# Performance work log

Hardware: AMD Instinct MI355X
Metric: run time of the kernel (lower is better)

## Reference

```python
import jax, jax.numpy as jnp
import numpy as np

N_NODES = 100000
N_EDGES = 3200000
D_FEAT = 512
HIDDEN = 16
N_CLASSES = 7


def setup_inputs() -> dict:
    key = jax.random.key(0)
    k1, k2, k3, k4 = jax.random.split(key, 4)
    x = jax.random.normal(k1, (N_NODES, D_FEAT), dtype=jnp.float32)
    edge_index = jax.random.randint(k2, (2, N_EDGES), 0, N_NODES, dtype=jnp.int64)
    # Glorot-ish scaled weights
    W1 = jax.random.normal(k3, (D_FEAT, HIDDEN), dtype=jnp.float32) * (1.0 / np.sqrt(D_FEAT))
    b1 = jnp.zeros((HIDDEN,), dtype=jnp.float32)
    W2 = jax.random.normal(k4, (HIDDEN, N_CLASSES), dtype=jnp.float32) * (1.0 / np.sqrt(HIDDEN))
    b2 = jnp.zeros((N_CLASSES,), dtype=jnp.float32)
    return {"x": x, "edge_index": edge_index, "W1": W1, "b1": b1, "W2": W2, "b2": b2}


def _gcn_norm(edge_index, num_nodes):
    # Add self-loops, then symmetric normalization: D^-1/2 A D^-1/2
    loop = jnp.arange(num_nodes, dtype=edge_index.dtype)
    src = jnp.concatenate([edge_index[0], loop])
    dst = jnp.concatenate([edge_index[1], loop])
    deg = jax.ops.segment_sum(jnp.ones_like(dst, dtype=jnp.float32), dst,
                              num_segments=num_nodes)
    dinv = jnp.where(deg > 0, jax.lax.rsqrt(deg), 0.0)
    w = dinv[src] * dinv[dst]  # [E+N]
    return src, dst, w


def _gcn_conv(x, W, b, src, dst, w, num_nodes):
    h = x @ W                               # transform first (small out dim)
    m = jax.ops.segment_sum(h[src] * w[:, None], dst, num_segments=num_nodes)
    return m + b


def reference(x, edge_index, W1, b1, W2, b2):
    n = x.shape[0]
    src, dst, w = _gcn_norm(edge_index, n)
    h = jax.nn.relu(_gcn_conv(x, W1, b1, src, dst, w, n))
    # dropout is identity at inference
    logits = _gcn_conv(h, W2, b2, src, dst, w, n)
    return jax.nn.log_softmax(logits, axis=1)
```

## Files before the change

### kernel.cpp

```cpp
#include <hip/hip_runtime.h>
#include <cmath>

#define N_NODES   100000
#define N_EDGES   3200000
#define D_FEAT    512
#define HIDDEN    16
#define N_CLASSES 7

#define NCHUNK 250
#define CHUNK  12800
#define NBKT   1563
#define NSCAN  (NBKT * NCHUNK)

typedef __attribute__((ext_vector_type(4))) float  f32x4;
typedef __attribute__((ext_vector_type(8))) short  bf16x8;

__device__ __forceinline__ short f2bf(float f) {
    union { float f; unsigned u; } v; v.f = f;
    unsigned r = v.u + 0x7fffu + ((v.u >> 16) & 1u);
    return (short)(r >> 16);
}
__device__ __forceinline__ float bf2f(unsigned short s) {
    union { unsigned u; float f; } v; v.u = ((unsigned)s) << 16;
    return v.f;
}

__global__ __launch_bounds__(1024) void k_hist1(const int* __restrict__ dst,
                                                unsigned* __restrict__ hist) {
    __shared__ unsigned h[NBKT];
    int t = threadIdx.x, b = blockIdx.x;
    for (int i = t; i < NBKT; i += 1024) h[i] = 0u;
    __syncthreads();
    int base = b * CHUNK;
    #pragma unroll 2
    for (int k = 0; k < 13; ++k) {
        int idx = k * 1024 + t;
        if (idx < CHUNK) atomicAdd(&h[((unsigned)dst[base + idx]) >> 6], 1u);
    }
    __syncthreads();
    for (int i = t; i < NBKT; i += 1024)
        hist[(size_t)i * NCHUNK + b] = h[i];
}

__global__ __launch_bounds__(256) void k_scan_a(unsigned* __restrict__ hist,
                                                unsigned* __restrict__ bin_total) {
    __shared__ unsigned t0[256];
    int t = threadIdx.x, b = blockIdx.x;
    unsigned v = (t < NCHUNK) ? hist[(size_t)b * NCHUNK + t] : 0u;
    t0[t] = v; __syncthreads();
    #pragma unroll
    for (int off = 1; off < 256; off <<= 1) {
        unsigned add = (t >= off) ? t0[t - off] : 0u;
        __syncthreads();
        t0[t] += add;
        __syncthreads();
    }
    if (t < NCHUNK) hist[(size_t)b * NCHUNK + t] = t0[t] - v;
    if (t == 255) bin_total[b] = t0[t];
}

__global__ __launch_bounds__(256) void k_scan_b(const unsigned* __restrict__ bin_total,
                                                unsigned* __restrict__ bin_base) {
    __shared__ unsigned t0[256];
    int t = threadIdx.x;
    unsigned running = 0u;
    for (int c0 = 0; c0 < NBKT; c0 += 256) {
        int i = c0 + t;
        unsigned v = (i < NBKT) ? bin_total[i] : 0u;
        t0[t] = v; __syncthreads();
        #pragma unroll
        for (int off = 1; off < 256; off <<= 1) {
            unsigned add = (t >= off) ? t0[t - off] : 0u;
            __syncthreads();
            t0[t] += add;
            __syncthreads();
        }
        if (i < NBKT) bin_base[i] = running + t0[t] - v;
        unsigned chunk_sum = t0[255];
        __syncthreads();
        running += chunk_sum;
    }
    if (t == 0) bin_base[NBKT] = running;
}

__global__ __launch_bounds__(1024) void k_scatter1(const int* __restrict__ src,
                                                   const int* __restrict__ dst,
                                                   const unsigned* __restrict__ hist,
                                                   const unsigned* __restrict__ bin_base,
                                                   unsigned* __restrict__ packed) {
    __shared__ unsigned cur[NBKT];
    int t = threadIdx.x, b = blockIdx.x;
    for (int i = t; i < NBKT; i += 1024)
        cur[i] = hist[(size_t)i * NCHUNK + b] + bin_base[i];
    __syncthreads();
    int base = b * CHUNK;
    #pragma unroll 2
    for (int k = 0; k < 13; ++k) {
        int idx = k * 1024 + t;
        if (idx < CHUNK) {
            int e = base + idx;
            unsigned d = (unsigned)dst[e];
            unsigned pos = atomicAdd(&cur[d >> 6], 1u);
            packed[pos] = ((d & 63u) << 24) | (unsigned)src[e];
        }
    }
}

__global__ __launch_bounds__(256) void k_bucket(const unsigned* __restrict__ packed,
                                                const unsigned* __restrict__ bin_base,
                                                unsigned* __restrict__ deg,
                                                unsigned* __restrict__ row_start,
                                                float* __restrict__ dinv,
                                                int* __restrict__ csr_src) {
    __shared__ unsigned hh[4][64], sc[64], cur[64];
    int t = threadIdx.x, b = blockIdx.x;
    int w = t >> 6, l = t & 63;
    unsigned rs = bin_base[b];
    unsigned re = bin_base[b + 1];
    hh[w][l] = 0u;
    __syncthreads();
    for (unsigned i = rs + t; i < re; i += 256)
        atomicAdd(&hh[w][packed[i] >> 24], 1u);
    __syncthreads();
    unsigned total = 0u;
    if (t < 64) {
        total = hh[0][t] + hh[1][t] + hh[2][t] + hh[3][t];
        sc[t] = total;
    }
    __syncthreads();
    #pragma unroll
    for (int off = 1; off < 64; off <<= 1) {
        unsigned add = (t >= off && t < 64) ? sc[t - off] : 0u;
        __syncthreads();
        if (t < 64) sc[t] += add;
        __syncthreads();
    }
    if (t < 64) {
        unsigned excl = sc[t] - total;
        int node = b * 64 + t;
        if (node < N_NODES) {
            deg[node]       = total;
            row_start[node] = rs + excl;
            dinv[node]      = rsqrtf((float)(total + 1u));
        }
        cur[t] = rs + excl;
    }
    __syncthreads();
    for (unsigned i = rs + t; i < re; i += 256) {
        unsigned p = packed[i];
        unsigned pos = atomicAdd(&cur[p >> 24], 1u);
        csr_src[pos] = (int)(p & 0xFFFFFFu);
    }
}

__global__ __launch_bounds__(256) void k_gemm1(const float* __restrict__ x,
                                               const float* __restrict__ w1,
                                               const float* __restrict__ dinv,
                                               unsigned short* __restrict__ h1p) {
    __shared__ __align__(16) short w1t[16][520];
    int tid = threadIdx.x;
    for (int idx = tid; idx < D_FEAT * HIDDEN; idx += 256) {
        int k = idx >> 4, n = idx & 15;
        w1t[n][k] = f2bf(w1[idx]);
    }
    __syncthreads();

    int lane = tid & 63, wid = tid >> 6;
    int m  = lane & 15;
    int kg = lane >> 4;

    bf16x8 bfrag[16];
    #pragma unroll
    for (int ks = 0; ks < 16; ++ks)
        bfrag[ks] = *(const bf16x8*)&w1t[m][ks * 32 + kg * 8];

    int tile = blockIdx.x * 4 + wid;
    if (tile >= (N_NODES / 16)) return;

    const f32x4* xr = (const f32x4*)(x + (size_t)(tile * 16 + m) * D_FEAT);
    f32x4 acc = {0.f, 0.f, 0.f, 0.f};
    #pragma unroll
    for (int ks = 0; ks < 16; ++ks) {
        f32x4 x0 = xr[ks * 8 + kg * 2];
        f32x4 x1 = xr[ks * 8 + kg * 2 + 1];
        bf16x8 a;
        a[0] = f2bf(x0[0]); a[1] = f2bf(x0[1]); a[2] = f2bf(x0[2]); a[3] = f2bf(x0[3]);
        a[4] = f2bf(x1[0]); a[5] = f2bf(x1[1]); a[6] = f2bf(x1[2]); a[7] = f2bf(x1[3]);
        acc = __builtin_amdgcn_mfma_f32_16x16x32_bf16(a, bfrag[ks], acc, 0, 0, 0);
    }
    size_t base = (size_t)tile * 256;
    #pragma unroll
    for (int r = 0; r < 4; ++r) {
        int rr = kg * 4 + r;
        h1p[base + rr * 16 + m] = (unsigned short)f2bf(dinv[tile * 16 + rr] * acc[r]);
    }
}

__global__ __launch_bounds__(256) void k_gather1(const int* __restrict__ csr_src,
                                                 const unsigned* __restrict__ row_start,
                                                 const unsigned* __restrict__ deg,
                                                 const unsigned short* __restrict__ h1p,
                                                 float* __restrict__ g1) {
    int tid  = threadIdx.x;
    int lane = tid & 63;
    int node = blockIdx.x * 4 + (tid >> 6);
    int j  = lane & 15;
    int sl = lane >> 4;

    unsigned start = row_start[node];
    unsigned end   = start + deg[node];

    float acc = (sl == 0) ? bf2f(h1p[(size_t)node * 16 + j]) : 0.f;
    unsigned e = start;
    for (; e + 16 <= end; e += 16) {
        int s0 = csr_src[e      + sl];
        int s1 = csr_src[e + 4  + sl];
        int s2 = csr_src[e + 8  + sl];
        int s3 = csr_src[e + 12 + sl];
        float v0 = bf2f(h1p[(size_t)s0 * 16 + j]);
        float v1 = bf2f(h1p[(size_t)s1 * 16 + j]);
        float v2 = bf2f(h1p[(size_t)s2 * 16 + j]);
        float v3 = bf2f(h1p[(size_t)s3 * 16 + j]);
        acc += v0; acc += v1; acc += v2; acc += v3;
    }
    for (; e < end; e += 4) {
        unsigned idx = e + (unsigned)sl;
        float v = 0.f;
        if (idx < end) v = bf2f(h1p[(size_t)csr_src[idx] * 16 + j]);
        acc += v;
    }
    acc += __shfl_down(acc, 32);
    acc += __shfl_down(acc, 16);
    if (sl == 0) g1[(size_t)node * 16 + j] = acc;
}

__global__ __launch_bounds__(256) void k_layer2(const float* __restrict__ g1,
                                                const float* __restrict__ dinv,
                                                const float* __restrict__ w2,
                                                const float* __restrict__ b1,
                                                float* __restrict__ h2p) {
    int i = blockIdx.x * 256 + threadIdx.x;
    if (i >= N_NODES) return;
    float di = dinv[i];
    const float* gr = g1 + (size_t)i * 16;
    float h[16];
    #pragma unroll
    for (int j = 0; j < 16; ++j) h[j] = fmaxf(di * gr[j] + b1[j], 0.f);
    float* h2r = h2p + (size_t)i * 8;
    #pragma unroll
    for (int c = 0; c < N_CLASSES; ++c) {
        float o = 0.f;
        #pragma unroll
        for (int j = 0; j < 16; ++j) o += h[j] * w2[j * N_CLASSES + c];
        h2r[c] = di * o;
    }
    h2r[7] = 0.f;
}

__global__ __launch_bounds__(256) void k_gather2(const int* __restrict__ csr_src,
                                                 const unsigned* __restrict__ row_start,
                                                 const unsigned* __restrict__ deg,
                                                 const float* __restrict__ dinv,
                                                 const float* __restrict__ h2p,
                                                 const float* __restrict__ b2,
                                                 float* __restrict__ out) {
    int tid  = threadIdx.x;
    int lane = tid & 63;
    int node = blockIdx.x * 4 + (tid >> 6);
    int j  = lane & 7;
    int sl = lane >> 3;

    unsigned start = row_start[node];
    unsigned end   = start + deg[node];

    float acc = (sl == 0) ? h2p[(size_t)node * 8 + j] : 0.f;
    unsigned e = start;
    for (; e + 32 <= end; e += 32) {
        int s0 = csr_src[e      + sl];
        int s1 = csr_src[e + 8  + sl];
        int s2 = csr_src[e + 16 + sl];
        int s3 = csr_src[e + 24 + sl];
        float v0 = h2p[(size_t)s0 * 8 + j];
        float v1 = h2p[(size_t)s1 * 8 + j];
        float v2 = h2p[(size_t)s2 * 8 + j];
        float v3 = h2p[(size_t)s3 * 8 + j];
        acc += v0; acc += v1; acc += v2; acc += v3;
    }
    for (; e < end; e += 8) {
        unsigned idx = e + (unsigned)sl;
        float v = 0.f;
        if (idx < end) v = h2p[(size_t)csr_src[idx] * 8 + j];
        acc += v;
    }
    acc += __shfl_down(acc, 32);
    acc += __shfl_down(acc, 16);
    acc += __shfl_down(acc, 8);
    float di = dinv[node];
    float logit = (j < N_CLASSES) ? di * acc + b2[j] : -1e30f;
    float mx = logit;
    #pragma unroll
    for (int mk = 1; mk < 8; mk <<= 1) mx = fmaxf(mx, __shfl_xor(mx, mk, 8));
    float ex = (j < N_CLASSES) ? __expf(logit - mx) : 0.f;
    float sum = ex;
    #pragma unroll
    for (int mk = 1; mk < 8; mk <<= 1) sum += __shfl_xor(sum, mk, 8);
    if (sl == 0 && j < N_CLASSES)
        out[(size_t)node * N_CLASSES + j] = logit - mx - __logf(sum);
}

extern "C" void kernel_launch(void* const* d_in, const int* in_sizes, int n_in,
                              void* d_out, int out_size, void* d_ws, size_t ws_size,
                              hipStream_t stream) {
    const float* x  = (const float*)d_in[0];
    const int*   ei = (const int*)d_in[1];
    const float* w1 = (const float*)d_in[2];
    const float* b1 = (const float*)d_in[3];
    const float* w2 = (const float*)d_in[4];
    const float* b2 = (const float*)d_in[5];
    float* out = (float*)d_out;

    const int* src = ei;
    const int* dst = ei + N_EDGES;

    unsigned* w32        = (unsigned*)d_ws;
    float*    dinv       = (float*)(w32 + 0);
    unsigned short* h1p  = (unsigned short*)(w32 + 102400);
    float*    g1         = (float*)(w32 + 902400);
    float*    h2p        = (float*)(w32 + 2502400);
    unsigned* deg        = w32 + 3302400;
    unsigned* row_start  = w32 + 3404800;
    unsigned* hist       = w32 + 3507200;
    unsigned* bin_total  = w32 + 3897984;
    unsigned* bin_base   = w32 + 3899552;
    unsigned* packed     = w32 + 3901120;
    int*      csr_src    = (int*)(w32 + 7101120);

    const int GB = (N_NODES / 16 + 3) / 4;

    k_hist1   <<<NCHUNK, 1024, 0, stream>>>(dst, hist);
    k_scan_a  <<<NBKT,   256,  0, stream>>>(hist, bin_total);
    k_scan_b  <<<1,      256,  0, stream>>>(bin_total, bin_base);
    k_scatter1<<<NCHUNK, 1024, 0, stream>>>(src, dst, hist, bin_base, packed);
    k_bucket  <<<NBKT,   256,  0, stream>>>(packed, bin_base, deg, row_start, dinv, csr_src);
    k_gemm1   <<<GB,     256,  0, stream>>>(x, w1, dinv, h1p);
    k_gather1 <<<25000,  256,  0, stream>>>(csr_src, row_start, deg, h1p, g1);
    k_layer2  <<<(N_NODES + 255) / 256, 256, 0, stream>>>(g1, dinv, w2, b1, h2p);
    k_gather2 <<<25000,  256,  0, stream>>>(csr_src, row_start, deg, dinv, h2p, b2, out);
}
```

Measured before the change: 490.8 us.

## Fuse layer-2 transform into gather1, store h2 as bf16, stage bucket in LDS

Folds the per-node ReLU and W2 projection into the first gather kernel, using a 16-lane shuffle reduction, and removes the separate k_layer2 launch along with the g1 intermediate. h2 is now written as packed bf16 (16 bytes per node), which halves the bytes gathered in the second aggregation at some cost in precision. k_bucket copies its bucket's packed entries into shared memory once instead of reading global memory twice. The gather loops drop their separate tail loops in favour of predicated full iterations.

Result: slower. 528.1 us (+7.6%).

```diff
diff --git a/kernel.cpp b/kernel.cpp
--- a/kernel.cpp
+++ b/kernel.cpp
@@ -10,7 +10,7 @@
 #define NCHUNK 250
 #define CHUNK  12800
 #define NBKT   1563
-#define NSCAN  (NBKT * NCHUNK)
+#define BCAP   4096
 
 typedef __attribute__((ext_vector_type(4))) float  f32x4;
 typedef __attribute__((ext_vector_type(8))) short  bf16x8;
@@ -112,15 +112,22 @@
                                                 unsigned* __restrict__ row_start,
                                                 float* __restrict__ dinv,
                                                 int* __restrict__ csr_src) {
+    __shared__ unsigned pbuf[BCAP];
     __shared__ unsigned hh[4][64], sc[64], cur[64];
     int t = threadIdx.x, b = blockIdx.x;
     int w = t >> 6, l = t & 63;
     unsigned rs = bin_base[b];
     unsigned re = bin_base[b + 1];
+    unsigned n  = re - rs;
+    bool fits = (n <= BCAP);
+    if (fits)
+        for (unsigned i = t; i < n; i += 256) pbuf[i] = packed[rs + i];
     hh[w][l] = 0u;
     __syncthreads();
-    for (unsigned i = rs + t; i < re; i += 256)
-        atomicAdd(&hh[w][packed[i] >> 24], 1u);
+    for (unsigned i = t; i < n; i += 256) {
+        unsigned p = fits ? pbuf[i] : packed[rs + i];
+        atomicAdd(&hh[w][p >> 24], 1u);
+    }
     __syncthreads();
     unsigned total = 0u;
     if (t < 64) {
@@ -146,8 +153,8 @@
         cur[t] = rs + excl;
     }
     __syncthreads();
-    for (unsigned i = rs + t; i < re; i += 256) {
-        unsigned p = packed[i];
+    for (unsigned i = t; i < n; i += 256) {
+        unsigned p = fits ? pbuf[i] : packed[rs + i];
         unsigned pos = atomicAdd(&cur[p >> 24], 1u);
         csr_src[pos] = (int)(p & 0xFFFFFFu);
     }
@@ -199,69 +206,68 @@
 __global__ __launch_bounds__(256) void k_gather1(const int* __restrict__ csr_src,
                                                  const unsigned* __restrict__ row_start,
                                                  const unsigned* __restrict__ deg,
+                                                 const float* __restrict__ dinv,
                                                  const unsigned short* __restrict__ h1p,
-                                                 float* __restrict__ g1) {
+                                                 const float* __restrict__ w2,
+                                                 const float* __restrict__ b1,
+                                                 unsigned short* __restrict__ h2p) {
     int tid  = threadIdx.x;
     int lane = tid & 63;
     int node = blockIdx.x * 4 + (tid >> 6);
     int j  = lane & 15;
     int sl = lane >> 4;
 
+    float b1j = b1[j];
+    float w2j[N_CLASSES];
+    #pragma unroll
+    for (int c = 0; c < N_CLASSES; ++c) w2j[c] = w2[j * N_CLASSES + c];
+
     unsigned start = row_start[node];
     unsigned end   = start + deg[node];
 
     float acc = (sl == 0) ? bf2f(h1p[(size_t)node * 16 + j]) : 0.f;
-    unsigned e = start;
-    for (; e + 16 <= end; e += 16) {
-        int s0 = csr_src[e      + sl];
-        int s1 = csr_src[e + 4  + sl];
-        int s2 = csr_src[e + 8  + sl];
-        int s3 = csr_src[e + 12 + sl];
-        float v0 = bf2f(h1p[(size_t)s0 * 16 + j]);
-        float v1 = bf2f(h1p[(size_t)s1 * 16 + j]);
-        float v2 = bf2f(h1p[(size_t)s2 * 16 + j]);
-        float v3 = bf2f(h1p[(size_t)s3 * 16 + j]);
+    for (unsigned e0 = start; e0 < end; e0 += 16) {
+        unsigned i0 = e0 + (unsigned)sl, i1 = i0 + 4, i2 = i0 + 8, i3 = i0 + 12;
+        int s0 = (i0 < end) ? csr_src[i0] : 0;
+        int s1 = (i1 < end) ? csr_src[i1] : 0;
+        int s2 = (i2 < end) ? csr_src[i2] : 0;
+        int s3 = (i3 < end) ? csr_src[i3] : 0;
+        float v0 = (i0 < end) ? bf2f(h1p[(size_t)s0 * 16 + j]) : 0.f;
+        float v1 = (i1 < end) ? bf2f(h1p[(size_t)s1 * 16 + j]) : 0.f;
+        float v2 = (i2 < end) ? bf2f(h1p[(size_t)s2 * 16 + j]) : 0.f;
+        float v3 = (i3 < end) ? bf2f(h1p[(size_t)s3 * 16 + j]) : 0.f;
         acc += v0; acc += v1; acc += v2; acc += v3;
-    }
-    for (; e < end; e += 4) {
-        unsigned idx = e + (unsigned)sl;
-        float v = 0.f;
-        if (idx < end) v = bf2f(h1p[(size_t)csr_src[idx] * 16 + j]);
-        acc += v;
     }
     acc += __shfl_down(acc, 32);
     acc += __shfl_down(acc, 16);
-    if (sl == 0) g1[(size_t)node * 16 + j] = acc;
-}
-
-__global__ __launch_bounds__(256) void k_layer2(const float* __restrict__ g1,
-                                                const float* __restrict__ dinv,
-                                                const float* __restrict__ w2,
-                                                const float* __restrict__ b1,
-                                                float* __restrict__ h2p) {
-    int i = blockIdx.x * 256 + threadIdx.x;
-    if (i >= N_NODES) return;
-    float di = dinv[i];
-    const float* gr = g1 + (size_t)i * 16;
-    float h[16];
-    #pragma unroll
-    for (int j = 0; j < 16; ++j) h[j] = fmaxf(di * gr[j] + b1[j], 0.f);
-    float* h2r = h2p + (size_t)i * 8;
-    #pragma unroll
-    for (int c = 0; c < N_CLASSES; ++c) {
-        float o = 0.f;
+    float di = dinv[node];
+    float h = fmaxf(di * acc + b1j, 0.f);
+    float s[N_CLASSES];
+    #pragma unroll
+    for (int c = 0; c < N_CLASSES; ++c) s[c] = h * w2j[c];
+    #pragma unroll
+    for (int mk = 1; mk < 16; mk <<= 1) {
         #pragma unroll
-        for (int j = 0; j < 16; ++j) o += h[j] * w2[j * N_CLASSES + c];
-        h2r[c] = di * o;
-    }
-    h2r[7] = 0.f;
+        for (int c = 0; c < N_CLASSES; ++c) s[c] += __shfl_xor(s[c], mk, 16);
+    }
+    if (lane == 0) {
+        unsigned u0 = (unsigned)(unsigned short)f2bf(di * s[0]) |
+                      ((unsigned)(unsigned short)f2bf(di * s[1]) << 16);
+        unsigned u1 = (unsigned)(unsigned short)f2bf(di * s[2]) |
+                      ((unsigned)(unsigned short)f2bf(di * s[3]) << 16);
+        unsigned u2 = (unsigned)(unsigned short)f2bf(di * s[4]) |
+                      ((unsigned)(unsigned short)f2bf(di * s[5]) << 16);
+        unsigned u3 = (unsigned)(unsigned short)f2bf(di * s[6]);
+        uint4 pk; pk.x = u0; pk.y = u1; pk.z = u2; pk.w = u3;
+        *(uint4*)(h2p + (size_t)node * 8) = pk;
+    }
 }
 
 __global__ __launch_bounds__(256) void k_gather2(const int* __restrict__ csr_src,
                                                  const unsigned* __restrict__ row_start,
                                                  const unsigned* __restrict__ deg,
                                                  const float* __restrict__ dinv,
-                                                 const float* __restrict__ h2p,
+                                                 const unsigned short* __restrict__ h2p,
                                                  const float* __restrict__ b2,
                                                  float* __restrict__ out) {
     int tid  = threadIdx.x;
@@ -273,24 +279,18 @@
     unsigned start = row_start[node];
     unsigned end   = start + deg[node];
 
-    float acc = (sl == 0) ? h2p[(size_t)node * 8 + j] : 0.f;
-    unsigned e = start;
-    for (; e + 32 <= end; e += 32) {
-        int s0 = csr_src[e      + sl];
-        int s1 = csr_src[e + 8  + sl];
-        int s2 = csr_src[e + 16 + sl];
-        int s3 = csr_src[e + 24 + sl];
-        float v0 = h2p[(size_t)s0 * 8 + j];
-        float v1 = h2p[(size_t)s1 * 8 + j];
-        float v2 = h2p[(size_t)s2 * 8 + j];
-        float v3 = h2p[(size_t)s3 * 8 + j];
+    float acc = (sl == 0) ? bf2f(h2p[(size_t)node * 8 + j]) : 0.f;
+    for (unsigned e0 = start; e0 < end; e0 += 32) {
+        unsigned i0 = e0 + (unsigned)sl, i1 = i0 + 8, i2 = i0 + 16, i3 = i0 + 24;
+        int s0 = (i0 < end) ? csr_src[i0] : 0;
+        int s1 = (i1 < end) ? csr_src[i1] : 0;
+        int s2 = (i2 < end) ? csr_src[i2] : 0;
+        int s3 = (i3 < end) ? csr_src[i3] : 0;
+        float v0 = (i0 < end) ? bf2f(h2p[(size_t)s0 * 8 + j]) : 0.f;
+        float v1 = (i1 < end) ? bf2f(h2p[(size_t)s1 * 8 + j]) : 0.f;
+        float v2 = (i2 < end) ? bf2f(h2p[(size_t)s2 * 8 + j]) : 0.f;
+        float v3 = (i3 < end) ? bf2f(h2p[(size_t)s3 * 8 + j]) : 0.f;
         acc += v0; acc += v1; acc += v2; acc += v3;
-    }
-    for (; e < end; e += 8) {
-        unsigned idx = e + (unsigned)sl;
-        float v = 0.f;
-        if (idx < end) v = h2p[(size_t)csr_src[idx] * 8 + j];
-        acc += v;
     }
     acc += __shfl_down(acc, 32);
     acc += __shfl_down(acc, 16);
@@ -325,15 +325,14 @@
     unsigned* w32        = (unsigned*)d_ws;
     float*    dinv       = (float*)(w32 + 0);
     unsigned short* h1p  = (unsigned short*)(w32 + 102400);
-    float*    g1         = (float*)(w32 + 902400);
-    float*    h2p        = (float*)(w32 + 2502400);
-    unsigned* deg        = w32 + 3302400;
-    unsigned* row_start  = w32 + 3404800;
-    unsigned* hist       = w32 + 3507200;
-    unsigned* bin_total  = w32 + 3897984;
-    unsigned* bin_base   = w32 + 3899552;
-    unsigned* packed     = w32 + 3901120;
-    int*      csr_src    = (int*)(w32 + 7101120);
+    unsigned short* h2p  = (unsigned short*)(w32 + 902400);
+    unsigned* deg        = w32 + 1302400;
+    unsigned* row_start  = w32 + 1404800;
+    unsigned* hist       = w32 + 1507200;
+    unsigned* bin_total  = w32 + 1897984;
+    unsigned* bin_base   = w32 + 1899552;
+    unsigned* packed     = w32 + 1901120;
+    int*      csr_src    = (int*)(w32 + 5101120);
 
     const int GB = (N_NODES / 16 + 3) / 4;
 
@@ -343,7 +342,6 @@
     k_scatter1<<<NCHUNK, 1024, 0, stream>>>(src, dst, hist, bin_base, packed);
     k_bucket  <<<NBKT,   256,  0, stream>>>(packed, bin_base, deg, row_start, dinv, csr_src);
     k_gemm1   <<<GB,     256,  0, stream>>>(x, w1, dinv, h1p);
-    k_gather1 <<<25000,  256,  0, stream>>>(csr_src, row_start, deg, h1p, g1);
-    k_layer2  <<<(N_NODES + 255) / 256, 256, 0, stream>>>(g1, dinv, w2, b1, h2p);
+    k_gather1 <<<25000,  256,  0, stream>>>(csr_src, row_start, deg, dinv, h1p, w2, b1, h2p);
     k_gather2 <<<25000,  256,  0, stream>>>(csr_src, row_start, deg, dinv, h2p, b2, out);
 }
```
